# Kernel tuning notes

Hardware: AMD Instinct MI355X
Metric: run time of the kernel (lower is better)

The kernel has to match this reference:

```python
import jax, jax.numpy as jnp
import numpy as np


def _patches(x, k, pad):
    # x: [B,C,H,W] -> [B,C,k*k,Ho,Wo]
    if pad:
        x = jnp.pad(x, ((0, 0), (0, 0), (pad, pad), (pad, pad)))
    B, C, H, W = x.shape
    Ho, Wo = H - k + 1, W - k + 1
    cols = [x[:, :, i:i + Ho, j:j + Wo] for i in range(k) for j in range(k)]
    return jnp.stack(cols, axis=2)


def _tropical_conv(x, w, pad, reduce_fn):
    # y[b,o,h,w] = sum_c reduce_k ( x_patch[b,c,k,h,w] + w[o,c,k] )
    k = w.shape[-1]
    p = _patches(x, k, pad)                                   # [B,C,KK,Ho,Wo]
    wf = w.reshape(w.shape[0], w.shape[1], k * k)             # [O,C,KK]
    s = p[:, None] + wf[None, :, :, :, None, None]            # [B,O,C,KK,Ho,Wo]
    return reduce_fn(s, axis=3).sum(axis=2)                   # [B,O,Ho,Wo]


def _avgpool2(x):
    B, C, H, W = x.shape
    return x.reshape(B, C, H // 2, 2, W // 2, 2).mean(axis=(3, 5))


def setup_inputs() -> dict:
    key = jax.random.key(0)
    ks = jax.random.split(key, 9)
    return {
        "input": jax.random.normal(ks[0], (256, 1, 28, 28), jnp.float32),
        "w1": jax.random.normal(ks[1], (6, 1, 5, 5), jnp.float32),
        "w2": jax.random.normal(ks[2], (16, 6, 5, 5), jnp.float32),
        "fw1": jax.random.normal(ks[3], (120, 400), jnp.float32) * 0.05,
        "fb1": jax.random.normal(ks[4], (120,), jnp.float32) * 0.05,
        "fw2": jax.random.normal(ks[5], (84, 120), jnp.float32) * 0.05,
        "fb2": jax.random.normal(ks[6], (84,), jnp.float32) * 0.05,
        "fw3": jax.random.normal(ks[7], (10, 84), jnp.float32) * 0.05,
        "fb3": jax.random.normal(ks[8], (10,), jnp.float32) * 0.05,
    }


def reference(input, w1, w2, fw1, fb1, fw2, fb2, fw3, fb3):
    x = _tropical_conv(input, w1, pad=2, reduce_fn=jnp.min)   # [B,6,28,28]
    x = _avgpool2(x)                                          # [B,6,14,14]
    x = _tropical_conv(x, w2, pad=0, reduce_fn=jnp.max)       # [B,16,10,10]
    x = _avgpool2(x)                                          # [B,16,5,5]
    x = x.reshape(x.shape[0], -1)                             # [B,400]
    x = jax.nn.relu(x @ fw1.T + fb1)
    x = jax.nn.relu(x @ fw2.T + fb2)
    return x @ fw3.T + fb3                                    # [B,10]
```

## Files before the change

### kernel.cpp

```cpp
#include <hip/hip_runtime.h>


#define POS_INF 1e30f

__global__ __launch_bounds__(1024, 4) void lenet_fused(
    const float* __restrict__ input,
    const float* __restrict__ w1,
    const float* __restrict__ w2,
    const float* __restrict__ fw1,
    const float* __restrict__ fb1,
    const float* __restrict__ fw2,
    const float* __restrict__ fb2,
    const float* __restrict__ fw3,
    const float* __restrict__ fb3,
    float* __restrict__ out)
{
    __shared__ float smem[13930];
    float* sW1 = smem;
    float* sW2 = smem + 150;
    float* sX1 = smem + 2550;
    float* sX2 = smem + 3726;
    float* sH1 = smem + 4126;
    float* sH2 = smem + 4246;
    float* A   = smem + 4330;
    float* sIn = A;
    float* sP1 = A + 1024;
    float* sP2 = A;

    const int tid = threadIdx.x;
    const int b = blockIdx.x;

    if (tid < 150) sW1[tid] = w1[tid];
    for (int i = tid; i < 2400; i += 1024) sW2[i] = w2[i];
    {
        int r = (tid >> 5) - 2, c = (tid & 31) - 2;
        float v = 0.f;
        if ((unsigned)r < 28u && (unsigned)c < 28u) v = input[b * 784 + r * 28 + c];
        sIn[tid] = v;
    }
    __syncthreads();

    if (tid < 672) {
        int o = tid / 112, rem = tid % 112, g = rem / 28, j0 = rem % 28;
        float w[25];
        #pragma unroll
        for (int k = 0; k < 25; ++k) w[k] = sW1[o * 25 + k];
        float acc[7];
        #pragma unroll
        for (int h = 0; h < 7; ++h) acc[h] = POS_INF;
        const float* xb = sIn + (7 * g) * 32 + j0;
        #pragma unroll
        for (int r = 0; r < 11; ++r) {
            float x0 = xb[r*32+0], x1 = xb[r*32+1], x2 = xb[r*32+2],
                  x3 = xb[r*32+3], x4 = xb[r*32+4];
            #pragma unroll
            for (int h = 0; h < 7; ++h) {
                if (h <= r && r <= h + 4) {
                    const int i = r - h;
                    acc[h] = fminf(acc[h], x0 + w[i*5+0]);
                    acc[h] = fminf(acc[h], x1 + w[i*5+1]);
                    acc[h] = fminf(acc[h], x2 + w[i*5+2]);
                    acc[h] = fminf(acc[h], x3 + w[i*5+3]);
                    acc[h] = fminf(acc[h], x4 + w[i*5+4]);
                }
            }
        }
        #pragma unroll
        for (int h = 0; h < 7; ++h)
            sP1[(o * 28 + 7 * g + h) * 28 + j0] = acc[h];
    }
    __syncthreads();

    for (int idx = tid; idx < 1176; idx += 1024) {
        int o = idx / 196, rem = idx % 196, ph = rem / 14, pw = rem % 14;
        const float* p = sP1 + (o * 28 + 2 * ph) * 28 + 2 * pw;
        sX1[idx] = 0.25f * (p[0] + p[1] + p[28] + p[29]);
    }
    __syncthreads();

    if (tid < 960) {
        int o2 = tid / 120, rem = tid % 120;
        int c = rem / 20, rem2 = rem % 20;
        int j0 = rem2 >> 1, half = rem2 & 1;
        const int h0 = half * 5;
        const int oa = 2 * o2, ob = oa + 1;
        float wa[25], wb[25];
        #pragma unroll
        for (int k = 0; k < 25; ++k) wa[k] = sW2[(oa * 6 + c) * 25 + k];
        #pragma unroll
        for (int k = 0; k < 25; ++k) wb[k] = sW2[(ob * 6 + c) * 25 + k];
        float aa[5], ab[5];
        #pragma unroll
        for (int h = 0; h < 5; ++h) { aa[h] = -POS_INF; ab[h] = -POS_INF; }
        const float* xb = sX1 + c * 196 + j0;
        #pragma unroll
        for (int r = 0; r < 9; ++r) {
            const int row = (h0 + r) * 14;
            float x0 = xb[row+0], x1 = xb[row+1], x2 = xb[row+2],
                  x3 = xb[row+3], x4 = xb[row+4];
            #pragma unroll
            for (int h = 0; h < 5; ++h) {
                if (h <= r && r <= h + 4) {
                    const int i = r - h;
                    aa[h] = fmaxf(aa[h], x0 + wa[i*5+0]);
                    aa[h] = fmaxf(aa[h], x1 + wa[i*5+1]);
                    aa[h] = fmaxf(aa[h], x2 + wa[i*5+2]);
                    aa[h] = fmaxf(aa[h], x3 + wa[i*5+3]);
                    aa[h] = fmaxf(aa[h], x4 + wa[i*5+4]);
                    ab[h] = fmaxf(ab[h], x0 + wb[i*5+0]);
                    ab[h] = fmaxf(ab[h], x1 + wb[i*5+1]);
                    ab[h] = fmaxf(ab[h], x2 + wb[i*5+2]);
                    ab[h] = fmaxf(ab[h], x3 + wb[i*5+3]);
                    ab[h] = fmaxf(ab[h], x4 + wb[i*5+4]);
                }
            }
        }
        float* da = sP2 + (oa * 6 + c) * 100 + j0;
        float* db = sP2 + (ob * 6 + c) * 100 + j0;
        #pragma unroll
        for (int h = 0; h < 5; ++h) {
            da[(h0 + h) * 10] = aa[h];
            db[(h0 + h) * 10] = ab[h];
        }
    }
    __syncthreads();

    if (tid < 400) {
        int o = tid / 25, rem = tid % 25, ph = rem / 5, pw = rem % 5;
        float s = 0.f;
        #pragma unroll
        for (int c = 0; c < 6; ++c) {
            const float* p = sP2 + (o * 6 + c) * 100 + (2 * ph) * 10 + 2 * pw;
            s += p[0] + p[1] + p[10] + p[11];
        }
        sX2[tid] = 0.25f * s;
    }
    __syncthreads();

    if (tid < 960) {
        int n = tid >> 3, s8 = tid & 7;
        const float* w = fw1 + n * 400 + s8 * 50;
        const float* x = sX2 + s8 * 50;
        float a = 0.f;
        #pragma unroll 10
        for (int k = 0; k < 50; ++k) a += x[k] * w[k];
        a += __shfl_xor(a, 1, 8);
        a += __shfl_xor(a, 2, 8);
        a += __shfl_xor(a, 4, 8);
        if (s8 == 0) sH1[n] = fmaxf(a + fb1[n], 0.f);
    }
    __syncthreads();

    if (tid < 336) {
        int n = tid >> 2, s4 = tid & 3;
        const float* w = fw2 + n * 120 + s4 * 30;
        const float* x = sH1 + s4 * 30;
        float a = 0.f;
        #pragma unroll 10
        for (int k = 0; k < 30; ++k) a += x[k] * w[k];
        a += __shfl_xor(a, 1, 4);
        a += __shfl_xor(a, 2, 4);
        if (s4 == 0) sH2[n] = fmaxf(a + fb2[n], 0.f);
    }
    __syncthreads();

    if (tid < 40) {
        int n = tid >> 2, s4 = tid & 3;
        const float* w = fw3 + n * 84 + s4 * 21;
        const float* x = sH2 + s4 * 21;
        float a = 0.f;
        #pragma unroll 7
        for (int k = 0; k < 21; ++k) a += x[k] * w[k];
        a += __shfl_xor(a, 1, 4);
        a += __shfl_xor(a, 2, 4);
        if (s4 == 0) out[b * 10 + n] = a + fb3[n];
    }
}

extern "C" void kernel_launch(void* const* d_in, const int* in_sizes, int n_in,
                              void* d_out, int out_size, void* d_ws, size_t ws_size,
                              hipStream_t stream) {
    const float* input = (const float*)d_in[0];
    const float* w1  = (const float*)d_in[1];
    const float* w2  = (const float*)d_in[2];
    const float* fw1 = (const float*)d_in[3];
    const float* fb1 = (const float*)d_in[4];
    const float* fw2 = (const float*)d_in[5];
    const float* fb2 = (const float*)d_in[6];
    const float* fw3 = (const float*)d_in[7];
    const float* fb3 = (const float*)d_in[8];
    float* out = (float*)d_out;

    lenet_fused<<<256, 1024, 0, stream>>>(input, w1, w2, fw1, fb1, fw2, fb2,
                                          fw3, fb3, out);
}
```

Measured before the change: 85.47 us.

## Fuse avgpool into conv1, widen per-thread outputs, vectorize LDS and FC loads

Conv1 now has each thread compute two adjacent columns over four rows and apply the 2x2 average pool in registers. This removes the sP1 buffer along with one pass and one barrier. Inputs and pooled activations are stored as two column-shifted copies with padded strides so float4 LDS loads stay aligned. Conv2 now computes two adjacent columns per thread, halving the thread count, and the FC layers use float4 global loads with fewer lanes per row. The changes add LDS usage, register pressure and duplicate stores, and drop the occupancy hint from the launch bounds.

```diff
diff --git a/kernel.cpp b/kernel.cpp
--- a/kernel.cpp
+++ b/kernel.cpp
@@ -3,7 +3,7 @@
 
 #define POS_INF 1e30f
 
-__global__ __launch_bounds__(1024, 4) void lenet_fused(
+__global__ __launch_bounds__(1024) void lenet_fused(
     const float* __restrict__ input,
     const float* __restrict__ w1,
     const float* __restrict__ w2,
@@ -15,112 +15,138 @@
     const float* __restrict__ fb3,
     float* __restrict__ out)
 {
-    __shared__ float smem[13930];
-    float* sW1 = smem;
-    float* sW2 = smem + 150;
-    float* sX1 = smem + 2550;
-    float* sX2 = smem + 3726;
-    float* sH1 = smem + 4126;
-    float* sH2 = smem + 4246;
-    float* A   = smem + 4330;
-    float* sIn = A;
-    float* sP1 = A + 1024;
-    float* sP2 = A;
+    __shared__ float smem[15760];
+    float* sW1p = smem;
+    float* sW2p = smem + 176;
+    float* sX1c = smem + 2864;
+    float* sX2  = smem + 5552;
+    float* sH1  = smem + 5952;
+    float* sH2  = smem + 6072;
+    float* A    = smem + 6160;
+    float* sIn  = A;
+    float* sP2  = A;
 
     const int tid = threadIdx.x;
     const int b = blockIdx.x;
 
-    if (tid < 150) sW1[tid] = w1[tid];
-    for (int i = tid; i < 2400; i += 1024) sW2[i] = w2[i];
+    if (tid < 150) sW1p[(tid / 25) * 28 + tid % 25] = w1[tid];
+    for (int i = tid; i < 2400; i += 1024)
+        sW2p[(i / 25) * 28 + (i % 25)] = w2[i];
     {
-        int r = (tid >> 5) - 2, c = (tid & 31) - 2;
-        float v = 0.f;
-        if ((unsigned)r < 28u && (unsigned)c < 28u) v = input[b * 784 + r * 28 + c];
-        sIn[tid] = v;
-    }
-    __syncthreads();
-
-    if (tid < 672) {
-        int o = tid / 112, rem = tid % 112, g = rem / 28, j0 = rem % 28;
+        int r = tid >> 5, cc = tid & 31;
+        const float* inb = input + b * 784;
+        float v0 = 0.f, v1 = 0.f;
+        if (r >= 2 && r < 30) {
+            if (cc >= 2 && cc < 30) v0 = inb[(r - 2) * 28 + (cc - 2)];
+            if (cc < 28)            v1 = inb[(r - 2) * 28 + cc];
+        }
+        sIn[tid] = v0;
+        sIn[1024 + tid] = v1;
+    }
+    __syncthreads();
+
+    if (tid < 588) {
+        int o = tid / 98, rem = tid % 98;
+        int g = rem / 14, jp = rem % 14;
+        const int J = 2 * jp;
+        const int s = J & 3;
+        const float* xbase = sIn + (s >> 1) * 1024 + (J - s);
         float w[25];
         #pragma unroll
-        for (int k = 0; k < 25; ++k) w[k] = sW1[o * 25 + k];
-        float acc[7];
-        #pragma unroll
-        for (int h = 0; h < 7; ++h) acc[h] = POS_INF;
-        const float* xb = sIn + (7 * g) * 32 + j0;
-        #pragma unroll
-        for (int r = 0; r < 11; ++r) {
-            float x0 = xb[r*32+0], x1 = xb[r*32+1], x2 = xb[r*32+2],
-                  x3 = xb[r*32+3], x4 = xb[r*32+4];
+        for (int q = 0; q < 6; ++q) {
+            float4 t = ((const float4*)(sW1p + o * 28))[q];
+            w[4*q] = t.x; w[4*q+1] = t.y; w[4*q+2] = t.z; w[4*q+3] = t.w;
+        }
+        w[24] = sW1p[o * 28 + 24];
+        float accA[4], accB[4];
+        #pragma unroll
+        for (int h = 0; h < 4; ++h) { accA[h] = POS_INF; accB[h] = POS_INF; }
+        #pragma unroll
+        for (int ir = 0; ir < 8; ++ir) {
+            const float* row = xbase + (4 * g + ir) * 32;
+            float4 xa = ((const float4*)row)[0];
+            float4 xb = ((const float4*)row)[1];
+            float x[8] = {xa.x, xa.y, xa.z, xa.w, xb.x, xb.y, xb.z, xb.w};
             #pragma unroll
-            for (int h = 0; h < 7; ++h) {
-                if (h <= r && r <= h + 4) {
-                    const int i = r - h;
-                    acc[h] = fminf(acc[h], x0 + w[i*5+0]);
-                    acc[h] = fminf(acc[h], x1 + w[i*5+1]);
-                    acc[h] = fminf(acc[h], x2 + w[i*5+2]);
-                    acc[h] = fminf(acc[h], x3 + w[i*5+3]);
-                    acc[h] = fminf(acc[h], x4 + w[i*5+4]);
+            for (int h = 0; h < 4; ++h) {
+                if (ir >= h && ir <= h + 4) {
+                    const int i = ir - h;
+                    #pragma unroll
+                    for (int j = 0; j < 5; ++j) {
+                        accA[h] = fminf(accA[h], x[j]     + w[i*5+j]);
+                        accB[h] = fminf(accB[h], x[j + 1] + w[i*5+j]);
+                    }
                 }
             }
         }
-        #pragma unroll
-        for (int h = 0; h < 7; ++h)
-            sP1[(o * 28 + 7 * g + h) * 28 + j0] = acc[h];
-    }
-    __syncthreads();
-
-    for (int idx = tid; idx < 1176; idx += 1024) {
-        int o = idx / 196, rem = idx % 196, ph = rem / 14, pw = rem % 14;
-        const float* p = sP1 + (o * 28 + 2 * ph) * 28 + 2 * pw;
-        sX1[idx] = 0.25f * (p[0] + p[1] + p[28] + p[29]);
-    }
-    __syncthreads();
-
-    if (tid < 960) {
-        int o2 = tid / 120, rem = tid % 120;
-        int c = rem / 20, rem2 = rem % 20;
-        int j0 = rem2 >> 1, half = rem2 & 1;
-        const int h0 = half * 5;
-        const int oa = 2 * o2, ob = oa + 1;
+        float p0 = 0.25f * (accA[0] + accB[0] + accA[1] + accB[1]);
+        float p1 = 0.25f * (accA[2] + accB[2] + accA[3] + accB[3]);
+        #pragma unroll
+        for (int ci = 0; ci < 2; ++ci) {
+            int col = jp - 2 * ci;
+            if (col >= 0) {
+                float* dst = sX1c + ci * 1344 + o * 224 + (2 * g) * 16 + col;
+                dst[0]  = p0;
+                dst[16] = p1;
+            }
+        }
+    }
+    __syncthreads();
+
+    if (tid < 480) {
+        int o2 = tid / 60, rem = tid % 60;
+        int c = rem / 10, r2 = rem % 10;
+        int jp = r2 >> 1, half = r2 & 1;
+        const int j0 = 2 * jp;
+        const int s = j0 & 3;
+        const int h0 = 5 * half;
+        const int oa = 2 * o2;
         float wa[25], wb[25];
         #pragma unroll
-        for (int k = 0; k < 25; ++k) wa[k] = sW2[(oa * 6 + c) * 25 + k];
-        #pragma unroll
-        for (int k = 0; k < 25; ++k) wb[k] = sW2[(ob * 6 + c) * 25 + k];
-        float aa[5], ab[5];
-        #pragma unroll
-        for (int h = 0; h < 5; ++h) { aa[h] = -POS_INF; ab[h] = -POS_INF; }
-        const float* xb = sX1 + c * 196 + j0;
+        for (int q = 0; q < 6; ++q) {
+            float4 t = ((const float4*)(sW2p + (oa * 6 + c) * 28))[q];
+            wa[4*q] = t.x; wa[4*q+1] = t.y; wa[4*q+2] = t.z; wa[4*q+3] = t.w;
+            float4 u = ((const float4*)(sW2p + ((oa + 1) * 6 + c) * 28))[q];
+            wb[4*q] = u.x; wb[4*q+1] = u.y; wb[4*q+2] = u.z; wb[4*q+3] = u.w;
+        }
+        wa[24] = sW2p[(oa * 6 + c) * 28 + 24];
+        wb[24] = sW2p[((oa + 1) * 6 + c) * 28 + 24];
+        float aa0[5], aa1[5], ab0[5], ab1[5];
+        #pragma unroll
+        for (int h = 0; h < 5; ++h) {
+            aa0[h] = -POS_INF; aa1[h] = -POS_INF;
+            ab0[h] = -POS_INF; ab1[h] = -POS_INF;
+        }
+        const float* xbase = sX1c + (s >> 1) * 1344 + c * 224 + (j0 - s);
         #pragma unroll
         for (int r = 0; r < 9; ++r) {
-            const int row = (h0 + r) * 14;
-            float x0 = xb[row+0], x1 = xb[row+1], x2 = xb[row+2],
-                  x3 = xb[row+3], x4 = xb[row+4];
+            const float* row = xbase + (h0 + r) * 16;
+            float4 xa = ((const float4*)row)[0];
+            float4 xb = ((const float4*)row)[1];
+            float x[8] = {xa.x, xa.y, xa.z, xa.w, xb.x, xb.y, xb.z, xb.w};
             #pragma unroll
             for (int h = 0; h < 5; ++h) {
-                if (h <= r && r <= h + 4) {
+                if (r >= h && r <= h + 4) {
                     const int i = r - h;
-                    aa[h] = fmaxf(aa[h], x0 + wa[i*5+0]);
-                    aa[h] = fmaxf(aa[h], x1 + wa[i*5+1]);
-                    aa[h] = fmaxf(aa[h], x2 + wa[i*5+2]);
-                    aa[h] = fmaxf(aa[h], x3 + wa[i*5+3]);
-                    aa[h] = fmaxf(aa[h], x4 + wa[i*5+4]);
-                    ab[h] = fmaxf(ab[h], x0 + wb[i*5+0]);
-                    ab[h] = fmaxf(ab[h], x1 + wb[i*5+1]);
-                    ab[h] = fmaxf(ab[h], x2 + wb[i*5+2]);
-                    ab[h] = fmaxf(ab[h], x3 + wb[i*5+3]);
-                    ab[h] = fmaxf(ab[h], x4 + wb[i*5+4]);
+                    #pragma unroll
+                    for (int j = 0; j < 5; ++j) {
+                        const float va = wa[i*5+j], vb = wb[i*5+j];
+                        aa0[h] = fmaxf(aa0[h], x[j]     + va);
+                        aa1[h] = fmaxf(aa1[h], x[j + 1] + va);
+                        ab0[h] = fmaxf(ab0[h], x[j]     + vb);
+                        ab1[h] = fmaxf(ab1[h], x[j + 1] + vb);
+                    }
                 }
             }
         }
         float* da = sP2 + (oa * 6 + c) * 100 + j0;
-        float* db = sP2 + (ob * 6 + c) * 100 + j0;
+        float* db = sP2 + ((oa + 1) * 6 + c) * 100 + j0;
         #pragma unroll
         for (int h = 0; h < 5; ++h) {
-            da[(h0 + h) * 10] = aa[h];
-            db[(h0 + h) * 10] = ab[h];
+            da[(h0 + h) * 10]     = aa0[h];
+            da[(h0 + h) * 10 + 1] = aa1[h];
+            db[(h0 + h) * 10]     = ab0[h];
+            db[(h0 + h) * 10 + 1] = ab1[h];
         }
     }
     __syncthreads();
@@ -130,37 +156,47 @@
         float s = 0.f;
         #pragma unroll
         for (int c = 0; c < 6; ++c) {
-            const float* p = sP2 + (o * 6 + c) * 100 + (2 * ph) * 10 + 2 * pw;
-            s += p[0] + p[1] + p[10] + p[11];
+            const float* p = sP2 + (o * 6 + c) * 100 + 2 * ph * 10 + 2 * pw;
+            float2 u = *(const float2*)p;
+            float2 v = *(const float2*)(p + 10);
+            s += u.x + u.y + v.x + v.y;
         }
         sX2[tid] = 0.25f * s;
     }
     __syncthreads();
 
-    if (tid < 960) {
-        int n = tid >> 3, s8 = tid & 7;
-        const float* w = fw1 + n * 400 + s8 * 50;
-        const float* x = sX2 + s8 * 50;
+    if (tid < 480) {
+        int n = tid >> 2, s4 = tid & 3;
+        const float4* wrow = (const float4*)(fw1 + n * 400);
+        const float4* xv = (const float4*)sX2;
         float a = 0.f;
-        #pragma unroll 10
-        for (int k = 0; k < 50; ++k) a += x[k] * w[k];
-        a += __shfl_xor(a, 1, 8);
-        a += __shfl_xor(a, 2, 8);
-        a += __shfl_xor(a, 4, 8);
-        if (s8 == 0) sH1[n] = fmaxf(a + fb1[n], 0.f);
-    }
-    __syncthreads();
-
-    if (tid < 336) {
-        int n = tid >> 2, s4 = tid & 3;
-        const float* w = fw2 + n * 120 + s4 * 30;
-        const float* x = sH1 + s4 * 30;
-        float a = 0.f;
-        #pragma unroll 10
-        for (int k = 0; k < 30; ++k) a += x[k] * w[k];
+        #pragma unroll
+        for (int i = 0; i < 25; ++i) {
+            int j = s4 + 4 * i;
+            float4 wv = wrow[j];
+            float4 x4 = xv[j];
+            a += wv.x * x4.x + wv.y * x4.y + wv.z * x4.z + wv.w * x4.w;
+        }
         a += __shfl_xor(a, 1, 4);
         a += __shfl_xor(a, 2, 4);
-        if (s4 == 0) sH2[n] = fmaxf(a + fb2[n], 0.f);
+        if (s4 == 0) sH1[n] = fmaxf(a + fb1[n], 0.f);
+    }
+    __syncthreads();
+
+    if (tid < 168) {
+        int n = tid >> 1, s2 = tid & 1;
+        const float4* wrow = (const float4*)(fw2 + n * 120);
+        const float4* xv = (const float4*)sH1;
+        float a = 0.f;
+        #pragma unroll
+        for (int i = 0; i < 15; ++i) {
+            int j = s2 + 2 * i;
+            float4 wv = wrow[j];
+            float4 x4 = xv[j];
+            a += wv.x * x4.x + wv.y * x4.y + wv.z * x4.z + wv.w * x4.w;
+        }
+        a += __shfl_xor(a, 1, 2);
+        if (s2 == 0) sH2[n] = fmaxf(a + fb2[n], 0.f);
     }
     __syncthreads();
 
```

After: 79.17 us. 7.4% less time.
